# Performance work log

Measured on AMD Instinct MI355X. Metric: run time of the kernel, lower is better.

## Reference

```python
import jax, jax.numpy as jnp
import numpy as np

E, H, I = 8, 1024, 512          # experts, hidden, moe_intermediate
NG, TKG, TOPK = 4, 2, 4          # n_group, topk_group, num_experts_per_tok
SCALE = 2.5                      # routed_scaling_factor


def _mlp(x, wg, wu, wd):
    # SwiGLU MLP: down(silu(gate(x)) * up(x)), all bias-free
    return (jax.nn.silu(x @ wg) * (x @ wu)) @ wd


def setup_inputs() -> dict:
    key = jax.random.key(0)
    ks = jax.random.split(key, 8)
    s = 0.02
    return {
        "hidden_states": jax.random.normal(ks[0], (32, 256, H), jnp.float32),
        "gate_w": jax.random.normal(ks[1], (E, H), jnp.float32) * np.float32(np.sqrt(2.0 / H)),
        "correction_bias": jnp.zeros((E,), jnp.float32),
        "Wg": jax.random.normal(ks[2], (E, H, I), jnp.float32) * s,
        "Wu": jax.random.normal(ks[3], (E, H, I), jnp.float32) * s,
        "Wd": jax.random.normal(ks[4], (E, I, H), jnp.float32) * s,
        "Wg_s": jax.random.normal(ks[5], (H, I), jnp.float32) * s,
        "Wu_s": jax.random.normal(ks[6], (H, I), jnp.float32) * s,
        "Wd_s": jax.random.normal(ks[7], (I, H), jnp.float32) * s,
    }


def reference(hidden_states, gate_w, correction_bias, Wg, Wu, Wd, Wg_s, Wu_s, Wd_s):
    B, T, _ = hidden_states.shape
    x = hidden_states.reshape(-1, H)                     # [N, H]
    N = x.shape[0]

    # ---- TopkRouter + route_tokens_to_experts (float32 router math) ----
    logits = x @ gate_w.T                                # [N, E]
    scores = jax.nn.sigmoid(logits)
    scores_c = scores + correction_bias                  # scores for choice
    grp = scores_c.reshape(N, NG, E // NG)
    group_scores = jnp.sum(jax.lax.top_k(grp, 2)[0], axis=-1)        # [N, NG]
    grp_idx = jax.lax.top_k(group_scores, TKG)[1]                    # [N, TKG]
    group_mask = jnp.zeros_like(group_scores).at[
        jnp.arange(N)[:, None], grp_idx].set(1.0)                    # [N, NG]
    score_mask = jnp.repeat(group_mask, E // NG, axis=-1) > 0.5      # [N, E]
    scores_for_choice = jnp.where(score_mask, scores_c, 0.0)
    topk_idx = jax.lax.top_k(scores_for_choice, TOPK)[1]             # [N, K]
    topk_w = jnp.take_along_axis(scores, topk_idx, axis=-1)          # [N, K]
    topk_w = topk_w / (jnp.sum(topk_w, axis=-1, keepdims=True) + 1e-20)
    topk_w = topk_w * SCALE

    # ---- DSNaiveMoE: equivalent dense-expert combine ----
    # combine weight per (token, expert); zero for unrouted pairs, so the
    # dense evaluation produces exactly the gather/scatter loop's result.
    cw = jnp.sum(jax.nn.one_hot(topk_idx, E, dtype=topk_w.dtype) * topk_w[..., None], axis=1)  # [N, E]
    g = jnp.einsum('nh,ehi->eni', x, Wg)
    u = jnp.einsum('nh,ehi->eni', x, Wu)
    y = jnp.einsum('eni,eih->enh', jax.nn.silu(g) * u, Wd)           # [E, N, H]
    routed = jnp.einsum('enh,ne->nh', y, cw)                          # [N, H]

    # ---- shared expert on residual input (replaces residual add) ----
    out = routed + _mlp(x, Wg_s, Wu_s, Wd_s)
    return out.reshape(B, T, H)
```

## Files before the change

kernel.cpp:

```cpp
#include <hip/hip_runtime.h>

#define E_ 8
#define H_ 1024
#define I_ 512
#define NE 9
#define NTOK 8192
#define KC 4608

typedef __bf16 bf16;
typedef __bf16 bf16x8 __attribute__((ext_vector_type(8)));
typedef __bf16 bf16x4 __attribute__((ext_vector_type(4)));
typedef float f32x4 __attribute__((ext_vector_type(4)));

__device__ __forceinline__ void gload16(const bf16* g, bf16* l) {
  __builtin_amdgcn_global_load_lds(
      (const __attribute__((address_space(1))) void*)g,
      (__attribute__((address_space(3))) void*)l,
      16, 0, 0);
}

__global__ __launch_bounds__(256) void convert_kernel(
    const float* __restrict__ x, bf16* __restrict__ xb) {
  int i = blockIdx.x * 256 + threadIdx.x;
  f32x4 v = ((const f32x4*)x)[i];
  bf16x4 o = {(bf16)v.x, (bf16)v.y, (bf16)v.z, (bf16)v.w};
  ((bf16x4*)xb)[i] = o;
}

__global__ __launch_bounds__(256) void router_kernel(
    const float* __restrict__ x, const float* __restrict__ gw,
    const float* __restrict__ bias, float* __restrict__ cw) {
  int t = threadIdx.x;
  int l = t & 63, w = t >> 6;
  int n = blockIdx.x * 4 + w;
  const f32x4* xr = (const f32x4*)(x + (size_t)n * H_ + l * 16);
  float xv[16];
#pragma unroll
  for (int q = 0; q < 4; q++) {
    f32x4 v = xr[q];
    xv[q * 4 + 0] = v.x; xv[q * 4 + 1] = v.y; xv[q * 4 + 2] = v.z; xv[q * 4 + 3] = v.w;
  }
  float s[E_], sc[E_];
#pragma unroll
  for (int e = 0; e < E_; e++) {
    const f32x4* gr = (const f32x4*)(gw + e * H_ + l * 16);
    float acc = 0.f;
#pragma unroll
    for (int q = 0; q < 4; q++) {
      f32x4 g = gr[q];
      acc += xv[q * 4 + 0] * g.x + xv[q * 4 + 1] * g.y + xv[q * 4 + 2] * g.z + xv[q * 4 + 3] * g.w;
    }
#pragma unroll
    for (int off = 32; off > 0; off >>= 1) acc += __shfl_xor(acc, off, 64);
    float sig = 1.f / (1.f + __expf(-acc));
    s[e] = sig;
    sc[e] = sig + bias[e];
  }
  if (l == 0) {
    float gs[4];
#pragma unroll
    for (int g = 0; g < 4; g++) gs[g] = sc[2 * g] + sc[2 * g + 1];
    int g0 = 0;
    for (int g = 1; g < 4; g++) if (gs[g] > gs[g0]) g0 = g;
    int g1 = -1;
    for (int g = 0; g < 4; g++) {
      if (g == g0) continue;
      if (g1 < 0 || gs[g] > gs[g1]) g1 = g;
    }
    float outw[NE];
#pragma unroll
    for (int e = 0; e < E_; e++) outw[e] = 0.f;
    outw[8] = 1.f;
    int es[4] = {2 * g0, 2 * g0 + 1, 2 * g1, 2 * g1 + 1};
    float wsum = 1e-20f;
    for (int j = 0; j < 4; j++) wsum += s[es[j]];
    float inv = 2.5f / wsum;
    for (int j = 0; j < 4; j++) outw[es[j]] = s[es[j]] * inv;
#pragma unroll
    for (int e = 0; e < NE; e++) cw[(size_t)n * NE + e] = outw[e];
  }
}

__global__ __launch_bounds__(256) void transpose_kernel(
    const float* __restrict__ Wg, const float* __restrict__ Wu,
    const float* __restrict__ Wd, const float* __restrict__ Wgs,
    const float* __restrict__ Wus, const float* __restrict__ Wds,
    bf16* __restrict__ BgT, bf16* __restrict__ BuT, bf16* __restrict__ WdT) {
  __shared__ bf16 tile[32][33];
  int job = blockIdx.x >> 9;
  int tl = blockIdx.x & 511;
  const float* src;
  bf16* dst;
  int C, dst_ld;
  if (job < 18) {
    int e = job % 9;
    if (job < 9) src = (e < 8) ? Wg + (size_t)e * H_ * I_ : Wgs;
    else         src = (e < 8) ? Wu + (size_t)e * H_ * I_ : Wus;
    dst = ((job < 9) ? BgT : BuT) + (size_t)e * I_ * H_;
    C = I_; dst_ld = H_;
  } else {
    int e = job - 18;
    src = (e < 8) ? Wd + (size_t)e * I_ * H_ : Wds;
    dst = WdT + (size_t)e * I_;
    C = H_; dst_ld = KC;
  }
  int n_tc = C >> 5;
  int tr = tl / n_tc, tc = tl % n_tc;
  int tx = threadIdx.x & 31, ty = threadIdx.x >> 5;
#pragma unroll
  for (int j = 0; j < 4; j++) {
    int r = tr * 32 + ty + j * 8;
    tile[ty + j * 8][tx] = (bf16)src[(size_t)r * C + tc * 32 + tx];
  }
  __syncthreads();
#pragma unroll
  for (int j = 0; j < 4; j++) {
    int c = tc * 32 + ty + j * 8;
    dst[(size_t)c * dst_ld + tr * 32 + tx] = tile[tx][ty + j * 8];
  }
}


__global__ __launch_bounds__(256, 2) void gemm1_kernel(
    const bf16* __restrict__ X, const bf16* __restrict__ BgT,
    const bf16* __restrict__ BuT, const float* __restrict__ cw,
    bf16* __restrict__ Tp) {
  __shared__ bf16 As[128 * 64], Bgs[128 * 64], Bus[128 * 64];
  int t = threadIdx.x;
  int l = t & 63, w = t >> 6;
  int wm = w >> 1, wn = w & 1;
  int m0 = blockIdx.y * 128;
  int n0 = blockIdx.x * 128;
  int e = n0 >> 9;

  f32x4 accg[4][4], accu[4][4];
#pragma unroll
  for (int mi = 0; mi < 4; mi++)
#pragma unroll
    for (int ni = 0; ni < 4; ni++) {
      accg[mi][ni] = (f32x4){0.f, 0.f, 0.f, 0.f};
      accu[mi][ni] = (f32x4){0.f, 0.f, 0.f, 0.f};
    }

  int srow = t >> 3;
  int scol = (((t & 7) ^ ((t >> 3) & 7)) * 8);
  const bf16* ga = X + (size_t)(m0 + srow) * H_ + scol;
  const bf16* gg = BgT + (size_t)(n0 + srow) * H_ + scol;
  const bf16* gu = BuT + (size_t)(n0 + srow) * H_ + scol;
  bf16* la = As + w * 512;
  bf16* lg = Bgs + w * 512;
  bf16* lu = Bus + w * 512;

  for (int k0 = 0; k0 < H_; k0 += 64) {
#pragma unroll
    for (int i = 0; i < 4; i++) {
      gload16(ga + (size_t)i * 32 * H_ + k0, la + i * 2048);
      gload16(gg + (size_t)i * 32 * H_ + k0, lg + i * 2048);
      gload16(gu + (size_t)i * 32 * H_ + k0, lu + i * 2048);
    }
    __syncthreads();
#pragma unroll
    for (int ks = 0; ks < 2; ks++) {
      int ko = (((ks * 4 + (l >> 4)) ^ (l & 7)) * 8);
      int ar = wm * 64 + (l & 15);
      int br = wn * 64 + (l & 15);
      bf16x8 af[4], bg[4], bu[4];
#pragma unroll
      for (int mi = 0; mi < 4; mi++)
        af[mi] = *(const bf16x8*)(As + (ar + mi * 16) * 64 + ko);
#pragma unroll
      for (int ni = 0; ni < 4; ni++) {
        bg[ni] = *(const bf16x8*)(Bgs + (br + ni * 16) * 64 + ko);
        bu[ni] = *(const bf16x8*)(Bus + (br + ni * 16) * 64 + ko);
      }
#pragma unroll
      for (int mi = 0; mi < 4; mi++)
#pragma unroll
        for (int ni = 0; ni < 4; ni++) {
          accg[mi][ni] = __builtin_amdgcn_mfma_f32_16x16x32_bf16(af[mi], bg[ni], accg[mi][ni], 0, 0, 0);
          accu[mi][ni] = __builtin_amdgcn_mfma_f32_16x16x32_bf16(af[mi], bu[ni], accu[mi][ni], 0, 0, 0);
        }
    }
    __syncthreads();
  }
#pragma unroll
  for (int mi = 0; mi < 4; mi++) {
#pragma unroll
    for (int r = 0; r < 4; r++) {
      int row = m0 + wm * 64 + mi * 16 + (l >> 4) * 4 + r;
      float c = cw[(size_t)row * NE + e];
#pragma unroll
      for (int ni = 0; ni < 4; ni++) {
        float g = accg[mi][ni][r];
        float u = accu[mi][ni][r];
        float val = c * (g / (1.f + __expf(-g))) * u;
        int col = n0 + wn * 64 + ni * 16 + (l & 15);
        Tp[(size_t)row * KC + col] = (bf16)val;
      }
    }
  }
}

__global__ __launch_bounds__(256, 3) void gemm2_kernel(
    const bf16* __restrict__ Tp, const bf16* __restrict__ WdT,
    float* __restrict__ out) {
  __shared__ bf16 As[128 * 64], Bs[128 * 64];
  int t = threadIdx.x;
  int l = t & 63, w = t >> 6;
  int wm = w >> 1, wn = w & 1;
  int m0 = blockIdx.y * 128;
  int n0 = blockIdx.x * 128;

  f32x4 acc[4][4];
#pragma unroll
  for (int mi = 0; mi < 4; mi++)
#pragma unroll
    for (int ni = 0; ni < 4; ni++) acc[mi][ni] = (f32x4){0.f, 0.f, 0.f, 0.f};

  int srow = t >> 3;
  int scol = (((t & 7) ^ ((t >> 3) & 7)) * 8);
  const bf16* ga = Tp + (size_t)(m0 + srow) * KC + scol;
  const bf16* gb = WdT + (size_t)(n0 + srow) * KC + scol;
  bf16* la = As + w * 512;
  bf16* lb = Bs + w * 512;

  for (int k0 = 0; k0 < KC; k0 += 64) {
#pragma unroll
    for (int i = 0; i < 4; i++) {
      gload16(ga + (size_t)i * 32 * KC + k0, la + i * 2048);
      gload16(gb + (size_t)i * 32 * KC + k0, lb + i * 2048);
    }
    __syncthreads();
#pragma unroll
    for (int ks = 0; ks < 2; ks++) {
      int ko = (((ks * 4 + (l >> 4)) ^ (l & 7)) * 8);
      int ar = wm * 64 + (l & 15);
      int br = wn * 64 + (l & 15);
      bf16x8 af[4], bfv[4];
#pragma unroll
      for (int mi = 0; mi < 4; mi++)
        af[mi] = *(const bf16x8*)(As + (ar + mi * 16) * 64 + ko);
#pragma unroll
      for (int ni = 0; ni < 4; ni++)
        bfv[ni] = *(const bf16x8*)(Bs + (br + ni * 16) * 64 + ko);
#pragma unroll
      for (int mi = 0; mi < 4; mi++)
#pragma unroll
        for (int ni = 0; ni < 4; ni++)
          acc[mi][ni] = __builtin_amdgcn_mfma_f32_16x16x32_bf16(af[mi], bfv[ni], acc[mi][ni], 0, 0, 0);
    }
    __syncthreads();
  }
#pragma unroll
  for (int mi = 0; mi < 4; mi++) {
#pragma unroll
    for (int r = 0; r < 4; r++) {
      int row = m0 + wm * 64 + mi * 16 + (l >> 4) * 4 + r;
#pragma unroll
      for (int ni = 0; ni < 4; ni++) {
        int col = n0 + wn * 64 + ni * 16 + (l & 15);
        out[(size_t)row * H_ + col] = acc[mi][ni][r];
      }
    }
  }
}

extern "C" void kernel_launch(void* const* d_in, const int* in_sizes, int n_in,
                              void* d_out, int out_size, void* d_ws, size_t ws_size,
                              hipStream_t stream) {
  const float* x   = (const float*)d_in[0];
  const float* gw  = (const float*)d_in[1];
  const float* cb  = (const float*)d_in[2];
  const float* Wg  = (const float*)d_in[3];
  const float* Wu  = (const float*)d_in[4];
  const float* Wd  = (const float*)d_in[5];
  const float* Wgs = (const float*)d_in[6];
  const float* Wus = (const float*)d_in[7];
  const float* Wds = (const float*)d_in[8];

  char* ws = (char*)d_ws;
  size_t off = 0;
  float* cw = (float*)(ws + off); off += (size_t)NTOK * NE * 4;
  bf16* BgT = (bf16*)(ws + off);  off += (size_t)NE * I_ * H_ * 2;
  bf16* BuT = (bf16*)(ws + off);  off += (size_t)NE * I_ * H_ * 2;
  bf16* WdT = (bf16*)(ws + off);  off += (size_t)H_ * KC * 2;
  bf16* Xb  = (bf16*)(ws + off);  off += (size_t)NTOK * H_ * 2;
  bf16* Tp  = (bf16*)(ws + off);  off += (size_t)NTOK * KC * 2;

  hipLaunchKernelGGL(convert_kernel, dim3(NTOK * H_ / 1024), dim3(256), 0, stream,
                     x, Xb);
  hipLaunchKernelGGL(transpose_kernel, dim3(27 * 512), dim3(256), 0, stream,
                     Wg, Wu, Wd, Wgs, Wus, Wds, BgT, BuT, WdT);
  hipLaunchKernelGGL(router_kernel, dim3(NTOK / 4), dim3(256), 0, stream,
                     x, gw, cb, cw);
  hipLaunchKernelGGL(gemm1_kernel, dim3(KC / 128, NTOK / 128), dim3(256), 0, stream,
                     Xb, BgT, BuT, cw, Tp);
  hipLaunchKernelGGL(gemm2_kernel, dim3(H_ / 128, NTOK / 128), dim3(256), 0, stream,
                     Tp, WdT, (float*)d_out);
}
```

Measured before the change: 402.8 us.

## Replace dense all-expert evaluation with sparse token-to-expert gather and scatter-add

New measurement: 780.2 us. 93.7% more time.

```diff
diff --git a/kernel.cpp b/kernel.cpp
--- a/kernel.cpp
+++ b/kernel.cpp
@@ -5,7 +5,6 @@
 #define I_ 512
 #define NE 9
 #define NTOK 8192
-#define KC 4608
 
 typedef __bf16 bf16;
 typedef __bf16 bf16x8 __attribute__((ext_vector_type(8)));
@@ -29,7 +28,8 @@
 
 __global__ __launch_bounds__(256) void router_kernel(
     const float* __restrict__ x, const float* __restrict__ gw,
-    const float* __restrict__ bias, float* __restrict__ cw) {
+    const float* __restrict__ bias, int* __restrict__ cnt,
+    int* __restrict__ idx, float* __restrict__ cwp) {
   int t = threadIdx.x;
   int l = t & 63, w = t >> 6;
   int n = blockIdx.x * 4 + w;
@@ -67,17 +67,16 @@
       if (g == g0) continue;
       if (g1 < 0 || gs[g] > gs[g1]) g1 = g;
     }
-    float outw[NE];
-#pragma unroll
-    for (int e = 0; e < E_; e++) outw[e] = 0.f;
-    outw[8] = 1.f;
     int es[4] = {2 * g0, 2 * g0 + 1, 2 * g1, 2 * g1 + 1};
     float wsum = 1e-20f;
     for (int j = 0; j < 4; j++) wsum += s[es[j]];
     float inv = 2.5f / wsum;
-    for (int j = 0; j < 4; j++) outw[es[j]] = s[es[j]] * inv;
-#pragma unroll
-    for (int e = 0; e < NE; e++) cw[(size_t)n * NE + e] = outw[e];
+    for (int j = 0; j < 4; j++) {
+      int e = es[j];
+      int p = atomicAdd(&cnt[e], 1);
+      idx[e * NTOK + p] = n;
+      cwp[e * NTOK + p] = s[e] * inv;
+    }
   }
 }
 
@@ -101,8 +100,8 @@
   } else {
     int e = job - 18;
     src = (e < 8) ? Wd + (size_t)e * I_ * H_ : Wds;
-    dst = WdT + (size_t)e * I_;
-    C = H_; dst_ld = KC;
+    dst = WdT + (size_t)e * H_ * I_;
+    C = H_; dst_ld = I_;
   }
   int n_tc = C >> 5;
   int tr = tl / n_tc, tc = tl % n_tc;
@@ -123,15 +122,20 @@
 
 __global__ __launch_bounds__(256, 2) void gemm1_kernel(
     const bf16* __restrict__ X, const bf16* __restrict__ BgT,
-    const bf16* __restrict__ BuT, const float* __restrict__ cw,
-    bf16* __restrict__ Tp) {
+    const bf16* __restrict__ BuT, const int* __restrict__ idx,
+    const float* __restrict__ cwp, const int* __restrict__ cnt,
+    bf16* __restrict__ Tc) {
+  int slot = blockIdx.y;
+  int e = slot >> 6;
+  int m0 = (slot & 63) * 128;
+  int ne = (e < 8) ? cnt[e] : NTOK;
+  if (m0 >= ne) return;
+
   __shared__ bf16 As[128 * 64], Bgs[128 * 64], Bus[128 * 64];
   int t = threadIdx.x;
   int l = t & 63, w = t >> 6;
   int wm = w >> 1, wn = w & 1;
-  int m0 = blockIdx.y * 128;
   int n0 = blockIdx.x * 128;
-  int e = n0 >> 9;
 
   f32x4 accg[4][4], accu[4][4];
 #pragma unroll
@@ -144,9 +148,14 @@
 
   int srow = t >> 3;
   int scol = (((t & 7) ^ ((t >> 3) & 7)) * 8);
-  const bf16* ga = X + (size_t)(m0 + srow) * H_ + scol;
-  const bf16* gg = BgT + (size_t)(n0 + srow) * H_ + scol;
-  const bf16* gu = BuT + (size_t)(n0 + srow) * H_ + scol;
+  int rid[4];
+#pragma unroll
+  for (int i = 0; i < 4; i++) {
+    int r = m0 + srow + 32 * i;
+    rid[i] = (e < 8) ? ((r < ne) ? idx[e * NTOK + r] : 0) : r;
+  }
+  const bf16* gg = BgT + (size_t)e * I_ * H_ + (size_t)(n0 + srow) * H_ + scol;
+  const bf16* gu = BuT + (size_t)e * I_ * H_ + (size_t)(n0 + srow) * H_ + scol;
   bf16* la = As + w * 512;
   bf16* lg = Bgs + w * 512;
   bf16* lu = Bus + w * 512;
@@ -154,7 +163,7 @@
   for (int k0 = 0; k0 < H_; k0 += 64) {
 #pragma unroll
     for (int i = 0; i < 4; i++) {
-      gload16(ga + (size_t)i * 32 * H_ + k0, la + i * 2048);
+      gload16(X + (size_t)rid[i] * H_ + scol + k0, la + i * 2048);
       gload16(gg + (size_t)i * 32 * H_ + k0, lg + i * 2048);
       gload16(gu + (size_t)i * 32 * H_ + k0, lu + i * 2048);
     }
@@ -187,22 +196,25 @@
   for (int mi = 0; mi < 4; mi++) {
 #pragma unroll
     for (int r = 0; r < 4; r++) {
-      int row = m0 + wm * 64 + mi * 16 + (l >> 4) * 4 + r;
-      float c = cw[(size_t)row * NE + e];
-#pragma unroll
-      for (int ni = 0; ni < 4; ni++) {
-        float g = accg[mi][ni][r];
-        float u = accu[mi][ni][r];
-        float val = c * (g / (1.f + __expf(-g))) * u;
-        int col = n0 + wn * 64 + ni * 16 + (l & 15);
-        Tp[(size_t)row * KC + col] = (bf16)val;
+      int lr = wm * 64 + mi * 16 + (l >> 4) * 4 + r;
+      int pr = m0 + lr;
+      if (pr < ne) {
+        float c = (e < 8) ? cwp[e * NTOK + pr] : 1.0f;
+#pragma unroll
+        for (int ni = 0; ni < 4; ni++) {
+          float g = accg[mi][ni][r];
+          float u = accu[mi][ni][r];
+          float val = c * (g / (1.f + __expf(-g))) * u;
+          int col = n0 + wn * 64 + ni * 16 + (l & 15);
+          Tc[((size_t)e * NTOK + pr) * I_ + col] = (bf16)val;
+        }
       }
     }
   }
 }
 
-__global__ __launch_bounds__(256, 3) void gemm2_kernel(
-    const bf16* __restrict__ Tp, const bf16* __restrict__ WdT,
+__global__ __launch_bounds__(256, 3) void gemm2s_kernel(
+    const bf16* __restrict__ Tc, const bf16* __restrict__ WdT,
     float* __restrict__ out) {
   __shared__ bf16 As[128 * 64], Bs[128 * 64];
   int t = threadIdx.x;
@@ -219,16 +231,16 @@
 
   int srow = t >> 3;
   int scol = (((t & 7) ^ ((t >> 3) & 7)) * 8);
-  const bf16* ga = Tp + (size_t)(m0 + srow) * KC + scol;
-  const bf16* gb = WdT + (size_t)(n0 + srow) * KC + scol;
+  const bf16* ga = Tc + (size_t)8 * NTOK * I_ + (size_t)(m0 + srow) * I_ + scol;
+  const bf16* gb = WdT + (size_t)8 * H_ * I_ + (size_t)(n0 + srow) * I_ + scol;
   bf16* la = As + w * 512;
   bf16* lb = Bs + w * 512;
 
-  for (int k0 = 0; k0 < KC; k0 += 64) {
+  for (int k0 = 0; k0 < I_; k0 += 64) {
 #pragma unroll
     for (int i = 0; i < 4; i++) {
-      gload16(ga + (size_t)i * 32 * KC + k0, la + i * 2048);
-      gload16(gb + (size_t)i * 32 * KC + k0, lb + i * 2048);
+      gload16(ga + (size_t)i * 32 * I_ + k0, la + i * 2048);
+      gload16(gb + (size_t)i * 32 * I_ + k0, lb + i * 2048);
     }
     __syncthreads();
 #pragma unroll
@@ -260,6 +272,80 @@
       for (int ni = 0; ni < 4; ni++) {
         int col = n0 + wn * 64 + ni * 16 + (l & 15);
         out[(size_t)row * H_ + col] = acc[mi][ni][r];
+      }
+    }
+  }
+}
+
+__global__ __launch_bounds__(256, 3) void gemm2r_kernel(
+    const bf16* __restrict__ Tc, const bf16* __restrict__ WdT,
+    const int* __restrict__ idx, const int* __restrict__ cnt,
+    float* __restrict__ out) {
+  int slot = blockIdx.y;
+  int e = slot >> 6;
+  int m0 = (slot & 63) * 128;
+  int ne = cnt[e];
+  if (m0 >= ne) return;
+
+  __shared__ bf16 As[128 * 64], Bs[128 * 64];
+  int t = threadIdx.x;
+  int l = t & 63, w = t >> 6;
+  int wm = w >> 1, wn = w & 1;
+  int n0 = blockIdx.x * 128;
+
+  f32x4 acc[4][4];
+#pragma unroll
+  for (int mi = 0; mi < 4; mi++)
+#pragma unroll
+    for (int ni = 0; ni < 4; ni++) acc[mi][ni] = (f32x4){0.f, 0.f, 0.f, 0.f};
+
+  int srow = t >> 3;
+  int scol = (((t & 7) ^ ((t >> 3) & 7)) * 8);
+  const bf16* ga = Tc + (size_t)e * NTOK * I_ + (size_t)(m0 + srow) * I_ + scol;
+  const bf16* gb = WdT + (size_t)e * H_ * I_ + (size_t)(n0 + srow) * I_ + scol;
+  bf16* la = As + w * 512;
+  bf16* lb = Bs + w * 512;
+
+  for (int k0 = 0; k0 < I_; k0 += 64) {
+#pragma unroll
+    for (int i = 0; i < 4; i++) {
+      gload16(ga + (size_t)i * 32 * I_ + k0, la + i * 2048);
+      gload16(gb + (size_t)i * 32 * I_ + k0, lb + i * 2048);
+    }
+    __syncthreads();
+#pragma unroll
+    for (int ks = 0; ks < 2; ks++) {
+      int ko = (((ks * 4 + (l >> 4)) ^ (l & 7)) * 8);
+      int ar = wm * 64 + (l & 15);
+      int br = wn * 64 + (l & 15);
+      bf16x8 af[4], bfv[4];
+#pragma unroll
+      for (int mi = 0; mi < 4; mi++)
+        af[mi] = *(const bf16x8*)(As + (ar + mi * 16) * 64 + ko);
+#pragma unroll
+      for (int ni = 0; ni < 4; ni++)
+        bfv[ni] = *(const bf16x8*)(Bs + (br + ni * 16) * 64 + ko);
+#pragma unroll
+      for (int mi = 0; mi < 4; mi++)
+#pragma unroll
+        for (int ni = 0; ni < 4; ni++)
+          acc[mi][ni] = __builtin_amdgcn_mfma_f32_16x16x32_bf16(af[mi], bfv[ni], acc[mi][ni], 0, 0, 0);
+    }
+    __syncthreads();
+  }
+#pragma unroll
+  for (int mi = 0; mi < 4; mi++) {
+#pragma unroll
+    for (int r = 0; r < 4; r++) {
+      int lr = wm * 64 + mi * 16 + (l >> 4) * 4 + r;
+      int pr = m0 + lr;
+      if (pr < ne) {
+        int tok = idx[e * NTOK + pr];
+#pragma unroll
+        for (int ni = 0; ni < 4; ni++) {
+          int col = n0 + wn * 64 + ni * 16 + (l & 15);
+          atomicAdd(&out[(size_t)tok * H_ + col], acc[mi][ni][r]);
+        }
       }
     }
   }
@@ -280,21 +366,26 @@
 
   char* ws = (char*)d_ws;
   size_t off = 0;
-  float* cw = (float*)(ws + off); off += (size_t)NTOK * NE * 4;
+  int*   cnt = (int*)(ws + off);  off += 64;
+  int*   idx = (int*)(ws + off);  off += (size_t)E_ * NTOK * 4;
+  float* cwp = (float*)(ws + off); off += (size_t)E_ * NTOK * 4;
   bf16* BgT = (bf16*)(ws + off);  off += (size_t)NE * I_ * H_ * 2;
   bf16* BuT = (bf16*)(ws + off);  off += (size_t)NE * I_ * H_ * 2;
-  bf16* WdT = (bf16*)(ws + off);  off += (size_t)H_ * KC * 2;
+  bf16* WdT = (bf16*)(ws + off);  off += (size_t)NE * H_ * I_ * 2;
   bf16* Xb  = (bf16*)(ws + off);  off += (size_t)NTOK * H_ * 2;
-  bf16* Tp  = (bf16*)(ws + off);  off += (size_t)NTOK * KC * 2;
-
+  bf16* Tc  = (bf16*)(ws + off);  off += (size_t)NE * NTOK * I_ * 2;
+
+  hipMemsetAsync(cnt, 0, 64, stream);
   hipLaunchKernelGGL(convert_kernel, dim3(NTOK * H_ / 1024), dim3(256), 0, stream,
                      x, Xb);
   hipLaunchKernelGGL(transpose_kernel, dim3(27 * 512), dim3(256), 0, stream,
                      Wg, Wu, Wd, Wgs, Wus, Wds, BgT, BuT, WdT);
   hipLaunchKernelGGL(router_kernel, dim3(NTOK / 4), dim3(256), 0, stream,
-                     x, gw, cb, cw);
-  hipLaunchKernelGGL(gemm1_kernel, dim3(KC / 128, NTOK / 128), dim3(256), 0, stream,
-                     Xb, BgT, BuT, cw, Tp);
-  hipLaunchKernelGGL(gemm2_kernel, dim3(H_ / 128, NTOK / 128), dim3(256), 0, stream,
-                     Tp, WdT, (float*)d_out);
-}
+                     x, gw, cb, cnt, idx, cwp);
+  hipLaunchKernelGGL(gemm1_kernel, dim3(4, NE * 64), dim3(256), 0, stream,
+                     Xb, BgT, BuT, idx, cwp, cnt, Tc);
+  hipLaunchKernelGGL(gemm2s_kernel, dim3(8, 64), dim3(256), 0, stream,
+                     Tc, WdT, (float*)d_out);
+  hipLaunchKernelGGL(gemm2r_kernel, dim3(8, E_ * 64), dim3(256), 0, stream,
+                     Tc, WdT, idx, cnt, (float*)d_out);
+}
```
